# Performance work log

Measured on AMD Instinct MI355X. Metric: run time of the kernel, lower is better.

The kernel has to match this reference:

```python
import jax, jax.numpy as jnp
import numpy as np

N = 100000   # nodes
E = 1600000  # edges
F_IN = 64    # input features
H = 64       # hidden channels
C = 40       # classes


def setup_inputs() -> dict:
    key = jax.random.key(0)
    k1, k2, k3, k4 = jax.random.split(key, 4)
    x = jax.random.normal(k1, (N, F_IN), dtype=jnp.float32)
    edge_index = jax.random.randint(k2, (2, E), 0, N, dtype=jnp.int64)
    W1 = jax.random.normal(k3, (F_IN, H), dtype=jnp.float32) / np.sqrt(F_IN)
    b1 = jnp.zeros((H,), dtype=jnp.float32)
    W2 = jax.random.normal(k4, (H, C), dtype=jnp.float32) / np.sqrt(H)
    b2 = jnp.zeros((C,), dtype=jnp.float32)
    return {"x": x, "edge_index": edge_index, "W1": W1, "b1": b1, "W2": W2, "b2": b2}


def gcn_conv(x, src, dst, W, b):
    """PyG-style GCNConv: self-loops + symmetric deg^{-1/2} normalization.
    src/dst already include self-loops. x: [N, Fin], W: [Fin, Fout]."""
    n = x.shape[0]
    deg = jax.ops.segment_sum(jnp.ones_like(dst, dtype=x.dtype), dst, num_segments=n)
    dinv = jnp.where(deg > 0, jax.lax.rsqrt(deg), jnp.zeros_like(deg))
    norm = dinv[src] * dinv[dst]          # [E+N]
    h = x @ W                             # transform first (Fin -> Fout)
    msg = h[src] * norm[:, None]          # gather + scale, [E+N, Fout]
    out = jax.ops.segment_sum(msg, dst, num_segments=n)  # scatter-add
    return out + b


def reference(x, edge_index, W1, b1, W2, b2):
    n = x.shape[0]
    loops = jnp.arange(n, dtype=edge_index.dtype)
    src = jnp.concatenate([edge_index[0], loops])
    dst = jnp.concatenate([edge_index[1], loops])
    h = jax.nn.relu(gcn_conv(x, src, dst, W1, b1))
    # F.dropout in eval mode (training=False) is identity
    out = gcn_conv(h, src, dst, W2, b2)
    return jax.nn.log_softmax(out, axis=1)
```

## Files before the change

### kernel.cpp

```cpp
#include <hip/hip_runtime.h>
#include <math.h>

#define F1 64
#define F2 40
#define NB 1024
#define TILE 4096
#define FCAP 3200

typedef unsigned int uint;
typedef __attribute__((ext_vector_type(8))) short s8v;
typedef __attribute__((ext_vector_type(4))) float f4v;

union U8 { s8v s; uint4 q; uint u[4]; };

__device__ inline unsigned short f2bf(float f) {
    unsigned u = __float_as_uint(f);
    unsigned r = (u + 0x7FFFu + ((u >> 16) & 1u)) >> 16;
    return (unsigned short)r;
}
__device__ inline uint packbf(float lo, float hi) {
    return (uint)f2bf(lo) | ((uint)f2bf(hi) << 16);
}
__device__ inline float bf_lo(uint u) { return __uint_as_float(u << 16); }
__device__ inline float bf_hi(uint u) { return __uint_as_float(u & 0xFFFF0000u); }

__device__ inline void split2(float a, float b, uint* hu, uint* lu) {
    unsigned short ha = f2bf(a), hb = f2bf(b);
    *hu = (uint)ha | ((uint)hb << 16);
    float ra = a - __uint_as_float((uint)ha << 16);
    float rb = b - __uint_as_float((uint)hb << 16);
    *lu = packbf(ra, rb);
}

__global__ __launch_bounds__(256) void k_bhist(const int* __restrict__ dst,
                                               int* __restrict__ bcnt, int e, int bsh) {
    __shared__ int h[NB];
    int tid = threadIdx.x;
    for (int i = tid; i < NB; i += 256) h[i] = 0;
    __syncthreads();
    int base = blockIdx.x * TILE;
    int lim = min(base + TILE, e);
    for (int i = base + tid; i < lim; i += 256) atomicAdd(&h[dst[i] >> bsh], 1);
    __syncthreads();
    for (int i = tid; i < NB; i += 256) if (h[i]) atomicAdd(&bcnt[i], h[i]);
}

__global__ __launch_bounds__(NB) void k_bscan(const int* __restrict__ bcnt,
                                              int* __restrict__ bptr, int* __restrict__ gcur,
                                              int* __restrict__ row_ptr, int n, int e) {
    __shared__ int sh[NB];
    int t = threadIdx.x;
    sh[t] = bcnt[t];
    __syncthreads();
    for (int off = 1; off < NB; off <<= 1) {
        int v = (t >= off) ? sh[t - off] : 0;
        __syncthreads();
        sh[t] += v;
        __syncthreads();
    }
    int ex = t ? sh[t - 1] : 0;
    bptr[t] = ex;
    gcur[t] = ex;
    if (t == NB - 1) bptr[NB] = sh[NB - 1];
    if (t == 0) row_ptr[n] = e;
}

__global__ __launch_bounds__(256) void k_bscatter(const int* __restrict__ src,
                                                  const int* __restrict__ dst,
                                                  int* gcur,
                                                  unsigned long long* __restrict__ pairs,
                                                  int e, int bsh) {
    __shared__ int lhist[NB];
    __shared__ int lstart[NB];
    __shared__ int delta[NB];
    __shared__ unsigned long long stage[TILE];
    int tid = threadIdx.x;
    for (int i = tid; i < NB; i += 256) lhist[i] = 0;
    __syncthreads();
    int base = blockIdx.x * TILE;
    int cnt = min(TILE, e - base);
    int sA[16], dA[16], rA[16];
#pragma unroll
    for (int k = 0; k < 16; ++k) {
        int i = base + k * 256 + tid;
        if (i < e) {
            sA[k] = src[i];
            dA[k] = dst[i];
            rA[k] = atomicAdd(&lhist[dA[k] >> bsh], 1);
        }
    }
    __syncthreads();
    if (tid < 64) {
        const int per = NB / 64;
        int v[per];
        int b0 = tid * per, s = 0;
#pragma unroll
        for (int j = 0; j < per; ++j) { v[j] = lhist[b0 + j]; s += v[j]; }
        int sc = s;
        for (int o = 1; o < 64; o <<= 1) { int u = __shfl_up(sc, o); if (tid >= o) sc += u; }
        int ex = sc - s;
#pragma unroll
        for (int j = 0; j < per; ++j) { lstart[b0 + j] = ex; ex += v[j]; }
    }
    __syncthreads();
    for (int i = tid; i < NB; i += 256) {
        int c = lhist[i];
        if (c) delta[i] = atomicAdd(&gcur[i], c) - lstart[i];
    }
    __syncthreads();
#pragma unroll
    for (int k = 0; k < 16; ++k) {
        int i = base + k * 256 + tid;
        if (i < e) {
            int b = dA[k] >> bsh;
            stage[lstart[b] + rA[k]] =
                ((unsigned long long)(unsigned)sA[k] << 32) | (unsigned)dA[k];
        }
    }
    __syncthreads();
    for (int p = tid; p < cnt; p += 256) {
        unsigned long long pr = stage[p];
        int b = ((int)(unsigned)pr) >> bsh;
        pairs[delta[b] + p] = pr;
    }
}

__global__ __launch_bounds__(256) void k_final(const unsigned long long* __restrict__ pairs,
                                               const int* __restrict__ bptr,
                                               int* __restrict__ srcs,
                                               int* __restrict__ row_ptr,
                                               float* __restrict__ dinv,
                                               int n, int bsh) {
    __shared__ int ldeg[128];
    __shared__ int lrow[128];
    __shared__ int lcur[128];
    __shared__ unsigned long long stg[FCAP];
    int b = blockIdx.x, tid = threadIdx.x;
    int beg = bptr[b], cnt = bptr[b + 1] - beg;
    int node0 = b << bsh;
    int bnodes = 1 << bsh;
    for (int i = tid; i < bnodes; i += 256) { ldeg[i] = 0; lcur[i] = 0; }
    bool fit = cnt <= FCAP;
    __syncthreads();
    if (fit) {
        for (int p = tid; p < cnt; p += 256) {
            unsigned long long pr = pairs[beg + p];
            stg[p] = pr;
            atomicAdd(&ldeg[((int)(unsigned)pr) - node0], 1);
        }
    } else {
        for (int p = tid; p < cnt; p += 256)
            atomicAdd(&ldeg[((int)(unsigned)pairs[beg + p]) - node0], 1);
    }
    __syncthreads();
    if (tid < 64) {
        int per = bnodes >> 6;
        int b0 = tid * per, s = 0;
        for (int j = 0; j < per; ++j) s += ldeg[b0 + j];
        int sc = s;
        for (int o = 1; o < 64; o <<= 1) { int u = __shfl_up(sc, o); if (tid >= o) sc += u; }
        int ex = sc - s;
        for (int j = 0; j < per; ++j) { lrow[b0 + j] = ex; ex += ldeg[b0 + j]; }
    }
    __syncthreads();
    for (int i = tid; i < bnodes; i += 256) {
        int node = node0 + i;
        if (node < n) {
            row_ptr[node] = beg + lrow[i];
            dinv[node] = rsqrtf((float)(ldeg[i] + 1));
        }
    }
    if (fit) {
        for (int p = tid; p < cnt; p += 256) {
            unsigned long long pr = stg[p];
            int dl = ((int)(unsigned)pr) - node0;
            int r = atomicAdd(&lcur[dl], 1);
            srcs[beg + lrow[dl] + r] = (int)(pr >> 32);
        }
    } else {
        for (int p = tid; p < cnt; p += 256) {
            unsigned long long pr = pairs[beg + p];
            int dl = ((int)(unsigned)pr) - node0;
            int r = atomicAdd(&lcur[dl], 1);
            srcs[beg + lrow[dl] + r] = (int)(pr >> 32);
        }
    }
}

__global__ __launch_bounds__(256) void k_wprep(const float* __restrict__ W1,
                                               const float* __restrict__ W2,
                                               uint4* __restrict__ wf1,
                                               uint4* __restrict__ wf2) {
    int g = blockIdx.x * 256 + threadIdx.x;
    if (g < 512) {
        int ks = g >> 8, ct = (g >> 6) & 3, l = g & 63;
        int c = 16 * ct + (l & 15);
        int kb = 32 * ks + 8 * (l >> 4);
        uint hu[4], lu[4];
#pragma unroll
        for (int i = 0; i < 4; ++i)
            split2(W1[(kb + 2 * i) * 64 + c], W1[(kb + 2 * i + 1) * 64 + c], &hu[i], &lu[i]);
        wf1[(size_t)(ks * 4 + ct) * 64 + l]       = make_uint4(hu[0], hu[1], hu[2], hu[3]);
        wf1[(size_t)((2 + ks) * 4 + ct) * 64 + l] = make_uint4(lu[0], lu[1], lu[2], lu[3]);
    } else if (g < 896) {
        int v = g - 512;
        int ks = v / 192, rem = v % 192;
        int ct = rem >> 6, l = rem & 63;
        int c = 16 * ct + (l & 15);
        int kb = 32 * ks + 8 * (l >> 4);
        uint hu[4], lu[4];
#pragma unroll
        for (int i = 0; i < 4; ++i) {
            float a = (c < 40) ? W2[(kb + 2 * i) * 40 + c] : 0.0f;
            float b = (c < 40) ? W2[(kb + 2 * i + 1) * 40 + c] : 0.0f;
            split2(a, b, &hu[i], &lu[i]);
        }
        wf2[(size_t)(ks * 3 + ct) * 64 + l]       = make_uint4(hu[0], hu[1], hu[2], hu[3]);
        wf2[(size_t)((2 + ks) * 3 + ct) * 64 + l] = make_uint4(lu[0], lu[1], lu[2], lu[3]);
    }
}

__global__ __launch_bounds__(256) void k_gemm1(const float* __restrict__ x,
                                               const uint4* __restrict__ wf1,
                                               const float* __restrict__ dinv,
                                               unsigned short* __restrict__ h, int n) {
    int w = threadIdx.x >> 6, l = threadIdx.x & 63;
    int node0 = blockIdx.x * 64 + w * 16;
    int ar = min(node0 + (l & 15), n - 1);
    const float* ap = x + (size_t)ar * 64 + 8 * (l >> 4);
    float4 a0 = *(const float4*)ap;
    float4 a1 = *(const float4*)(ap + 4);
    float4 a2 = *(const float4*)(ap + 32);
    float4 a3 = *(const float4*)(ap + 36);
    U8 ah0, al0, ah1, al1;
    split2(a0.x, a0.y, &ah0.u[0], &al0.u[0]);
    split2(a0.z, a0.w, &ah0.u[1], &al0.u[1]);
    split2(a1.x, a1.y, &ah0.u[2], &al0.u[2]);
    split2(a1.z, a1.w, &ah0.u[3], &al0.u[3]);
    split2(a2.x, a2.y, &ah1.u[0], &al1.u[0]);
    split2(a2.z, a2.w, &ah1.u[1], &al1.u[1]);
    split2(a3.x, a3.y, &ah1.u[2], &al1.u[2]);
    split2(a3.z, a3.w, &ah1.u[3], &al1.u[3]);
    f4v acc[4];
#pragma unroll
    for (int ct = 0; ct < 4; ++ct) acc[ct] = (f4v){0.0f, 0.0f, 0.0f, 0.0f};
#pragma unroll
    for (int ct = 0; ct < 4; ++ct) {
        U8 bh0, bh1, bl0, bl1;
        bh0.q = wf1[(size_t)(0 * 4 + ct) * 64 + l];
        bh1.q = wf1[(size_t)(1 * 4 + ct) * 64 + l];
        bl0.q = wf1[(size_t)(2 * 4 + ct) * 64 + l];
        bl1.q = wf1[(size_t)(3 * 4 + ct) * 64 + l];
        acc[ct] = __builtin_amdgcn_mfma_f32_16x16x32_bf16(ah0.s, bh0.s, acc[ct], 0, 0, 0);
        acc[ct] = __builtin_amdgcn_mfma_f32_16x16x32_bf16(ah1.s, bh1.s, acc[ct], 0, 0, 0);
        acc[ct] = __builtin_amdgcn_mfma_f32_16x16x32_bf16(al0.s, bh0.s, acc[ct], 0, 0, 0);
        acc[ct] = __builtin_amdgcn_mfma_f32_16x16x32_bf16(al1.s, bh1.s, acc[ct], 0, 0, 0);
        acc[ct] = __builtin_amdgcn_mfma_f32_16x16x32_bf16(ah0.s, bl0.s, acc[ct], 0, 0, 0);
        acc[ct] = __builtin_amdgcn_mfma_f32_16x16x32_bf16(ah1.s, bl1.s, acc[ct], 0, 0, 0);
    }
    int r0 = node0 + (l >> 4) * 4;
    float dv[4];
#pragma unroll
    for (int r = 0; r < 4; ++r) dv[r] = dinv[min(r0 + r, n - 1)];
#pragma unroll
    for (int ct = 0; ct < 4; ++ct)
#pragma unroll
        for (int r = 0; r < 4; ++r)
            if (r0 + r < n)
                h[(size_t)(r0 + r) * 64 + 16 * ct + (l & 15)] = f2bf(acc[ct][r] * dv[r]);
}

__global__ __launch_bounds__(256) void k_gather(const uint4* __restrict__ h4,
                                                const int* __restrict__ srcs,
                                                const int* __restrict__ row_ptr,
                                                const float* __restrict__ dinv,
                                                const float* __restrict__ b,
                                                uint4* __restrict__ aggb, int n) {
    int node = (int)(((long long)blockIdx.x * 256 + threadIdx.x) >> 5);
    int lane = threadIdx.x & 63;
    int l32 = lane & 31;
    int hw = lane & 32;
    if (node >= n) return;
    int slot = l32 >> 3, j = l32 & 7;
    int e0 = row_ptr[node], cnt = row_ptr[node + 1] - e0;
    int idx = (l32 < cnt) ? srcs[e0 + l32] : 0;
    float a0x=0,a0y=0,a1x=0,a1y=0,a2x=0,a2y=0,a3x=0,a3y=0;
    if (slot == 0) {
        uint4 u = h4[(size_t)node * 8 + j];
        a0x = bf_lo(u.x); a0y = bf_hi(u.x);
        a1x = bf_lo(u.y); a1y = bf_hi(u.y);
        a2x = bf_lo(u.z); a2y = bf_hi(u.z);
        a3x = bf_lo(u.w); a3y = bf_hi(u.w);
    }
    int cl = max(min(cnt, 32) - 1, 0);
#pragma unroll
    for (int i = 0; i < 8; ++i) {
        int e = slot + 4 * i;
        int sv = __shfl(idx, hw + min(e, cl));
        uint4 u = h4[(size_t)sv * 8 + j];
        if (e < cnt) {
            a0x += bf_lo(u.x);  a0y += bf_hi(u.x);
            a1x += bf_lo(u.y);  a1y += bf_hi(u.y);
            a2x += bf_lo(u.z);  a2y += bf_hi(u.z);
            a3x += bf_lo(u.w);  a3y += bf_hi(u.w);
        }
    }
    for (int p = 32 + slot; p < cnt; p += 4) {
        int s0 = srcs[e0 + p];
        uint4 u0 = h4[(size_t)s0 * 8 + j];
        a0x += bf_lo(u0.x);  a0y += bf_hi(u0.x);
        a1x += bf_lo(u0.y);  a1y += bf_hi(u0.y);
        a2x += bf_lo(u0.z);  a2y += bf_hi(u0.z);
        a3x += bf_lo(u0.w);  a3y += bf_hi(u0.w);
    }
#define COMB(o) \
    a0x += __shfl_xor(a0x, o); a0y += __shfl_xor(a0y, o); \
    a1x += __shfl_xor(a1x, o); a1y += __shfl_xor(a1y, o); \
    a2x += __shfl_xor(a2x, o); a2y += __shfl_xor(a2y, o); \
    a3x += __shfl_xor(a3x, o); a3y += __shfl_xor(a3y, o);
    COMB(8) COMB(16)
#undef COMB
    if (slot == 0) {
        float di = dinv[node];
        float4 bl = *(const float4*)&b[8 * j];
        float4 bh = *(const float4*)&b[8 * j + 4];
        float v0 = fmaxf(fmaf(a0x, di, bl.x), 0.0f);
        float v1 = fmaxf(fmaf(a0y, di, bl.y), 0.0f);
        float v2 = fmaxf(fmaf(a1x, di, bl.z), 0.0f);
        float v3 = fmaxf(fmaf(a1y, di, bl.w), 0.0f);
        float v4 = fmaxf(fmaf(a2x, di, bh.x), 0.0f);
        float v5 = fmaxf(fmaf(a2y, di, bh.y), 0.0f);
        float v6 = fmaxf(fmaf(a3x, di, bh.z), 0.0f);
        float v7 = fmaxf(fmaf(a3y, di, bh.w), 0.0f);
        uint4 r;
        r.x = packbf(v0, v1); r.y = packbf(v2, v3);
        r.z = packbf(v4, v5); r.w = packbf(v6, v7);
        aggb[(size_t)node * 8 + j] = r;
    }
}

__global__ __launch_bounds__(256) void k_trans2(const uint4* __restrict__ aggb,
                                                const uint4* __restrict__ wf2,
                                                const float* __restrict__ dinv,
                                                unsigned short* __restrict__ t, int n) {
    int w = threadIdx.x >> 6, l = threadIdx.x & 63;
    int node0 = blockIdx.x * 64 + w * 16;
    int ar = min(node0 + (l & 15), n - 1);
    U8 a0, a1;
    a0.q = aggb[(size_t)ar * 8 + 0 + (l >> 4)];
    a1.q = aggb[(size_t)ar * 8 + 4 + (l >> 4)];
    f4v acc[3];
#pragma unroll
    for (int ct = 0; ct < 3; ++ct) acc[ct] = (f4v){0.0f, 0.0f, 0.0f, 0.0f};
#pragma unroll
    for (int ct = 0; ct < 3; ++ct) {
        U8 bh0, bh1, bl0, bl1;
        bh0.q = wf2[(size_t)(0 * 3 + ct) * 64 + l];
        bh1.q = wf2[(size_t)(1 * 3 + ct) * 64 + l];
        bl0.q = wf2[(size_t)(2 * 3 + ct) * 64 + l];
        bl1.q = wf2[(size_t)(3 * 3 + ct) * 64 + l];
        acc[ct] = __builtin_amdgcn_mfma_f32_16x16x32_bf16(a0.s, bh0.s, acc[ct], 0, 0, 0);
        acc[ct] = __builtin_amdgcn_mfma_f32_16x16x32_bf16(a1.s, bh1.s, acc[ct], 0, 0, 0);
        acc[ct] = __builtin_amdgcn_mfma_f32_16x16x32_bf16(a0.s, bl0.s, acc[ct], 0, 0, 0);
        acc[ct] = __builtin_amdgcn_mfma_f32_16x16x32_bf16(a1.s, bl1.s, acc[ct], 0, 0, 0);
    }
    int r0 = node0 + (l >> 4) * 4;
    float dv[4];
#pragma unroll
    for (int r = 0; r < 4; ++r) dv[r] = dinv[min(r0 + r, n - 1)];
#pragma unroll
    for (int ct = 0; ct < 3; ++ct) {
        int col = 16 * ct + (l & 15);
#pragma unroll
        for (int r = 0; r < 4; ++r)
            if (col < 40 && r0 + r < n)
                t[(size_t)(r0 + r) * 40 + col] = f2bf(acc[ct][r] * dv[r]);
    }
}

__global__ __launch_bounds__(256) void k_gather40(const uint2* __restrict__ t2,
                                                  const int* __restrict__ srcs,
                                                  const int* __restrict__ row_ptr,
                                                  const float* __restrict__ dinv,
                                                  const float* __restrict__ b2,
                                                  float* __restrict__ out, int n) {
    int node = (int)(((long long)blockIdx.x * 256 + threadIdx.x) >> 5);
    int lane = threadIdx.x & 63;
    int l32 = lane & 31;
    int hw = lane & 32;
    if (node >= n) return;
    int slot = l32 / 10;
    int j = l32 - slot * 10;
    int e0 = row_ptr[node];
    int cnt = row_ptr[node + 1] - e0;
    int idx = (l32 < cnt && l32 < 30) ? srcs[e0 + l32] : 0;
    float a0=0, a1=0, a2=0, a3=0;
    if (slot == 0) {
        uint2 u = t2[(size_t)node * 10 + j];
        a0 = bf_lo(u.x); a1 = bf_hi(u.x);
        a2 = bf_lo(u.y); a3 = bf_hi(u.y);
    }
    if (slot < 3) {
        int cl = max(min(cnt, 30) - 1, 0);
#pragma unroll
        for (int i = 0; i < 10; ++i) {
            int e = slot + 3 * i;
            int sv = __shfl(idx, hw + min(e, cl));
            uint2 u = t2[(size_t)sv * 10 + j];
            if (e < cnt) {
                a0 += bf_lo(u.x);  a1 += bf_hi(u.x);
                a2 += bf_lo(u.y);  a3 += bf_hi(u.y);
            }
        }
        for (int p = 30 + slot; p < cnt; p += 3) {
            int s0 = srcs[e0 + p];
            uint2 u0 = t2[(size_t)s0 * 10 + j];
            a0 += bf_lo(u0.x);  a1 += bf_hi(u0.x);
            a2 += bf_lo(u0.y);  a3 += bf_hi(u0.y);
        }
    }
    float t0 = a0 + __shfl(a0, lane + 10) + __shfl(a0, lane + 20);
    float t1 = a1 + __shfl(a1, lane + 10) + __shfl(a1, lane + 20);
    float t2s = a2 + __shfl(a2, lane + 10) + __shfl(a2, lane + 20);
    float t3 = a3 + __shfl(a3, lane + 10) + __shfl(a3, lane + 20);
    bool actc = l32 < 10;
    float di = dinv[node];
    float4 bb = actc ? *(const float4*)&b2[4 * l32] : make_float4(0, 0, 0, 0);
    float v0 = fmaf(t0, di, bb.x);
    float v1 = fmaf(t1, di, bb.y);
    float v2 = fmaf(t2s, di, bb.z);
    float v3 = fmaf(t3, di, bb.w);
    float mv = actc ? fmaxf(fmaxf(v0, v1), fmaxf(v2, v3)) : -INFINITY;
    for (int o = 16; o; o >>= 1) mv = fmaxf(mv, __shfl_xor(mv, o));
    float ex = actc ? (expf(v0 - mv) + expf(v1 - mv) + expf(v2 - mv) + expf(v3 - mv)) : 0.0f;
    float s = ex;
    for (int o = 16; o; o >>= 1) s += __shfl_xor(s, o);
    float ls = mv + logf(s);
    if (actc) {
        float4 r = make_float4(v0 - ls, v1 - ls, v2 - ls, v3 - ls);
        *(float4*)&out[(size_t)node * 40 + 4 * l32] = r;
    }
}

extern "C" void kernel_launch(void* const* d_in, const int* in_sizes, int n_in,
                              void* d_out, int out_size, void* d_ws, size_t ws_size,
                              hipStream_t stream) {
    const float* x  = (const float*)d_in[0];
    const int*   ei = (const int*)d_in[1];
    const float* W1 = (const float*)d_in[2];
    const float* b1 = (const float*)d_in[3];
    const float* W2 = (const float*)d_in[4];
    const float* b2 = (const float*)d_in[5];

    const int N = in_sizes[0] / F1;
    const int E = in_sizes[1] / 2;
    const int* src = ei;
    const int* dst = ei + E;

    int bsh = 7;
    while ((((N - 1) >> bsh) + 1) > NB) ++bsh;
    const int NBu = ((N - 1) >> bsh) + 1;

    uint4* h1b     = (uint4*)d_ws;
    uint4* aggb    = h1b + (size_t)N * 8;
    uint2* tb      = (uint2*)(aggb + (size_t)N * 8);
    uint4* wf1     = (uint4*)(tb + (size_t)N * 10);
    uint4* wf2     = wf1 + 1024;
    unsigned long long* pairs = (unsigned long long*)(wf2 + 768);
    int*   srcs    = (int*)(pairs + E);
    int*   row_ptr = srcs + E;
    float* dinv    = (float*)(row_ptr + N + 1);
    int*   bcnt    = (int*)(dinv + N);
    int*   bptr    = bcnt + NB;
    int*   gcur    = bptr + NB + 1;
    float* outp    = (float*)d_out;

    const int B = 256;
    const int GT = (E + TILE - 1) / TILE;

    k_wprep<<<4, B, 0, stream>>>(W1, W2, wf1, wf2);

    hipMemsetAsync(bcnt, 0, NB * sizeof(int), stream);
    k_bhist<<<GT, B, 0, stream>>>(dst, bcnt, E, bsh);
    k_bscan<<<1, NB, 0, stream>>>(bcnt, bptr, gcur, row_ptr, N, E);
    k_bscatter<<<GT, B, 0, stream>>>(src, dst, gcur, pairs, E, bsh);
    k_final<<<NBu, B, 0, stream>>>(pairs, bptr, srcs, row_ptr, dinv, N, bsh);

    const int GM = (N + 63) / 64;

    k_gemm1<<<GM, B, 0, stream>>>(x, wf1, dinv, (unsigned short*)h1b, N);
    k_gather<<<(N + 7) / 8, B, 0, stream>>>(h1b, srcs, row_ptr, dinv, b1, aggb, N);

    k_trans2<<<GM, B, 0, stream>>>(aggb, wf2, dinv, (unsigned short*)tb, N);
    k_gather40<<<(N + 7) / 8, B, 0, stream>>>(tb, srcs, row_ptr, dinv, b2, outp, N);
}
```

Before: 238.6 us.

## Replace two-pass bucket sort CSR build with atomic-degree counting scatter

The CSR construction no longer does a bucketed radix-style scatter of packed (src,dst) pairs followed by a per-bucket local sort. Instead, the histogram pass also counts per-node degree with global atomics, a small kernel computes row pointers and cursors per node, and a flat kernel places each source with a global atomicAdd on its destination cursor. This removes the 64-bit pairs buffer and a full extra read and write of the edge list. In exchange it adds about 1.6M global atomics on the degree pass and again on the scatter, writes into srcs in random order, and leaves neighbour order within a row nondeterministic, which can change the floating-point summation order.

```diff
diff --git a/kernel.cpp b/kernel.cpp
--- a/kernel.cpp
+++ b/kernel.cpp
@@ -5,7 +5,6 @@
 #define F2 40
 #define NB 1024
 #define TILE 4096
-#define FCAP 3200
 
 typedef unsigned int uint;
 typedef __attribute__((ext_vector_type(8))) short s8v;
@@ -32,21 +31,26 @@
     *lu = packbf(ra, rb);
 }
 
-__global__ __launch_bounds__(256) void k_bhist(const int* __restrict__ dst,
-                                               int* __restrict__ bcnt, int e, int bsh) {
+__global__ __launch_bounds__(256) void k_bhist2(const int* __restrict__ dst,
+                                                int* __restrict__ bcnt,
+                                                int* __restrict__ deg, int e, int bsh) {
     __shared__ int h[NB];
     int tid = threadIdx.x;
     for (int i = tid; i < NB; i += 256) h[i] = 0;
     __syncthreads();
     int base = blockIdx.x * TILE;
     int lim = min(base + TILE, e);
-    for (int i = base + tid; i < lim; i += 256) atomicAdd(&h[dst[i] >> bsh], 1);
+    for (int i = base + tid; i < lim; i += 256) {
+        int d = dst[i];
+        atomicAdd(&h[d >> bsh], 1);
+        atomicAdd(&deg[d], 1);
+    }
     __syncthreads();
     for (int i = tid; i < NB; i += 256) if (h[i]) atomicAdd(&bcnt[i], h[i]);
 }
 
 __global__ __launch_bounds__(NB) void k_bscan(const int* __restrict__ bcnt,
-                                              int* __restrict__ bptr, int* __restrict__ gcur,
+                                              int* __restrict__ bptr,
                                               int* __restrict__ row_ptr, int n, int e) {
     __shared__ int sh[NB];
     int t = threadIdx.x;
@@ -58,132 +62,50 @@
         sh[t] += v;
         __syncthreads();
     }
-    int ex = t ? sh[t - 1] : 0;
-    bptr[t] = ex;
-    gcur[t] = ex;
+    bptr[t] = t ? sh[t - 1] : 0;
     if (t == NB - 1) bptr[NB] = sh[NB - 1];
     if (t == 0) row_ptr[n] = e;
 }
 
-__global__ __launch_bounds__(256) void k_bscatter(const int* __restrict__ src,
-                                                  const int* __restrict__ dst,
-                                                  int* gcur,
-                                                  unsigned long long* __restrict__ pairs,
-                                                  int e, int bsh) {
-    __shared__ int lhist[NB];
-    __shared__ int lstart[NB];
-    __shared__ int delta[NB];
-    __shared__ unsigned long long stage[TILE];
-    int tid = threadIdx.x;
-    for (int i = tid; i < NB; i += 256) lhist[i] = 0;
-    __syncthreads();
-    int base = blockIdx.x * TILE;
-    int cnt = min(TILE, e - base);
-    int sA[16], dA[16], rA[16];
-#pragma unroll
-    for (int k = 0; k < 16; ++k) {
-        int i = base + k * 256 + tid;
-        if (i < e) {
-            sA[k] = src[i];
-            dA[k] = dst[i];
-            rA[k] = atomicAdd(&lhist[dA[k] >> bsh], 1);
-        }
-    }
+__global__ __launch_bounds__(128) void k_rowptr(const int* __restrict__ deg,
+                                                const int* __restrict__ bptr,
+                                                int* __restrict__ row_ptr,
+                                                int* __restrict__ cur,
+                                                float* __restrict__ dinv, int n, int bsh) {
+    __shared__ int ldeg[128];
+    __shared__ int lrow[128];
+    int b = blockIdx.x, tid = threadIdx.x;
+    int node0 = b << bsh;
+    int node = node0 + tid;
+    ldeg[tid] = (node < n) ? deg[node] : 0;
     __syncthreads();
     if (tid < 64) {
-        const int per = NB / 64;
-        int v[per];
-        int b0 = tid * per, s = 0;
-#pragma unroll
-        for (int j = 0; j < per; ++j) { v[j] = lhist[b0 + j]; s += v[j]; }
+        int v0 = ldeg[2 * tid], v1 = ldeg[2 * tid + 1];
+        int s = v0 + v1;
         int sc = s;
         for (int o = 1; o < 64; o <<= 1) { int u = __shfl_up(sc, o); if (tid >= o) sc += u; }
         int ex = sc - s;
-#pragma unroll
-        for (int j = 0; j < per; ++j) { lstart[b0 + j] = ex; ex += v[j]; }
+        lrow[2 * tid] = ex;
+        lrow[2 * tid + 1] = ex + v0;
     }
     __syncthreads();
-    for (int i = tid; i < NB; i += 256) {
-        int c = lhist[i];
-        if (c) delta[i] = atomicAdd(&gcur[i], c) - lstart[i];
-    }
-    __syncthreads();
-#pragma unroll
-    for (int k = 0; k < 16; ++k) {
-        int i = base + k * 256 + tid;
-        if (i < e) {
-            int b = dA[k] >> bsh;
-            stage[lstart[b] + rA[k]] =
-                ((unsigned long long)(unsigned)sA[k] << 32) | (unsigned)dA[k];
-        }
-    }
-    __syncthreads();
-    for (int p = tid; p < cnt; p += 256) {
-        unsigned long long pr = stage[p];
-        int b = ((int)(unsigned)pr) >> bsh;
-        pairs[delta[b] + p] = pr;
-    }
-}
-
-__global__ __launch_bounds__(256) void k_final(const unsigned long long* __restrict__ pairs,
-                                               const int* __restrict__ bptr,
-                                               int* __restrict__ srcs,
-                                               int* __restrict__ row_ptr,
-                                               float* __restrict__ dinv,
-                                               int n, int bsh) {
-    __shared__ int ldeg[128];
-    __shared__ int lrow[128];
-    __shared__ int lcur[128];
-    __shared__ unsigned long long stg[FCAP];
-    int b = blockIdx.x, tid = threadIdx.x;
-    int beg = bptr[b], cnt = bptr[b + 1] - beg;
-    int node0 = b << bsh;
-    int bnodes = 1 << bsh;
-    for (int i = tid; i < bnodes; i += 256) { ldeg[i] = 0; lcur[i] = 0; }
-    bool fit = cnt <= FCAP;
-    __syncthreads();
-    if (fit) {
-        for (int p = tid; p < cnt; p += 256) {
-            unsigned long long pr = pairs[beg + p];
-            stg[p] = pr;
-            atomicAdd(&ldeg[((int)(unsigned)pr) - node0], 1);
-        }
-    } else {
-        for (int p = tid; p < cnt; p += 256)
-            atomicAdd(&ldeg[((int)(unsigned)pairs[beg + p]) - node0], 1);
-    }
-    __syncthreads();
-    if (tid < 64) {
-        int per = bnodes >> 6;
-        int b0 = tid * per, s = 0;
-        for (int j = 0; j < per; ++j) s += ldeg[b0 + j];
-        int sc = s;
-        for (int o = 1; o < 64; o <<= 1) { int u = __shfl_up(sc, o); if (tid >= o) sc += u; }
-        int ex = sc - s;
-        for (int j = 0; j < per; ++j) { lrow[b0 + j] = ex; ex += ldeg[b0 + j]; }
-    }
-    __syncthreads();
-    for (int i = tid; i < bnodes; i += 256) {
-        int node = node0 + i;
-        if (node < n) {
-            row_ptr[node] = beg + lrow[i];
-            dinv[node] = rsqrtf((float)(ldeg[i] + 1));
-        }
-    }
-    if (fit) {
-        for (int p = tid; p < cnt; p += 256) {
-            unsigned long long pr = stg[p];
-            int dl = ((int)(unsigned)pr) - node0;
-            int r = atomicAdd(&lcur[dl], 1);
-            srcs[beg + lrow[dl] + r] = (int)(pr >> 32);
-        }
-    } else {
-        for (int p = tid; p < cnt; p += 256) {
-            unsigned long long pr = pairs[beg + p];
-            int dl = ((int)(unsigned)pr) - node0;
-            int r = atomicAdd(&lcur[dl], 1);
-            srcs[beg + lrow[dl] + r] = (int)(pr >> 32);
-        }
+    if (node < n) {
+        int rp = bptr[b] + lrow[tid];
+        row_ptr[node] = rp;
+        cur[node] = rp;
+        dinv[node] = rsqrtf((float)(ldeg[tid] + 1));
+    }
+}
+
+__global__ __launch_bounds__(256) void k_scatter(const int* __restrict__ src,
+                                                 const int* __restrict__ dst,
+                                                 int* __restrict__ cur,
+                                                 int* __restrict__ srcs, int e) {
+    int i = blockIdx.x * 256 + threadIdx.x;
+    if (i < e) {
+        int s = src[i], d = dst[i];
+        int pos = atomicAdd(&cur[d], 1);
+        srcs[pos] = s;
     }
 }
 
@@ -466,13 +388,13 @@
     uint2* tb      = (uint2*)(aggb + (size_t)N * 8);
     uint4* wf1     = (uint4*)(tb + (size_t)N * 10);
     uint4* wf2     = wf1 + 1024;
-    unsigned long long* pairs = (unsigned long long*)(wf2 + 768);
-    int*   srcs    = (int*)(pairs + E);
+    int*   srcs    = (int*)(wf2 + 768);
     int*   row_ptr = srcs + E;
     float* dinv    = (float*)(row_ptr + N + 1);
     int*   bcnt    = (int*)(dinv + N);
-    int*   bptr    = bcnt + NB;
-    int*   gcur    = bptr + NB + 1;
+    int*   deg     = bcnt + NB;
+    int*   cur     = deg + N;
+    int*   bptr    = cur + N;
     float* outp    = (float*)d_out;
 
     const int B = 256;
@@ -480,11 +402,11 @@
 
     k_wprep<<<4, B, 0, stream>>>(W1, W2, wf1, wf2);
 
-    hipMemsetAsync(bcnt, 0, NB * sizeof(int), stream);
-    k_bhist<<<GT, B, 0, stream>>>(dst, bcnt, E, bsh);
-    k_bscan<<<1, NB, 0, stream>>>(bcnt, bptr, gcur, row_ptr, N, E);
-    k_bscatter<<<GT, B, 0, stream>>>(src, dst, gcur, pairs, E, bsh);
-    k_final<<<NBu, B, 0, stream>>>(pairs, bptr, srcs, row_ptr, dinv, N, bsh);
+    hipMemsetAsync(bcnt, 0, (NB + N) * sizeof(int), stream);
+    k_bhist2<<<GT, B, 0, stream>>>(dst, bcnt, deg, E, bsh);
+    k_bscan<<<1, NB, 0, stream>>>(bcnt, bptr, row_ptr, N, E);
+    k_rowptr<<<NBu, 128, 0, stream>>>(deg, bptr, row_ptr, cur, dinv, N, bsh);
+    k_scatter<<<(E + B - 1) / B, B, 0, stream>>>(src, dst, cur, srcs, E);
 
     const int GM = (N + 63) / 64;
 
```

Result: slower. 375.7 us (+57.4%).

## Fuse layer-1 gather with layer-2 transform via shared-memory staging

Applied to the files above, without the earlier changes.

Merges the layer-1 neighbor aggregation kernel and the layer-2 MFMA transform into one kernel. Each 256-thread block now aggregates 64 nodes over 8 rounds into a padded LDS tile, then runs the bf16 MFMA against W2 directly from LDS. This removes the global write and re-read of the intermediate aggregate and one kernel launch. In exchange, each block does its gather serially over rounds with a barrier before the transform, and it has 8x fewer blocks, which may reduce memory-level parallelism for the latency-bound gather.

```diff
diff --git a/kernel.cpp b/kernel.cpp
--- a/kernel.cpp
+++ b/kernel.cpp
@@ -270,85 +270,89 @@
                 h[(size_t)(r0 + r) * 64 + 16 * ct + (l & 15)] = f2bf(acc[ct][r] * dv[r]);
 }
 
-__global__ __launch_bounds__(256) void k_gather(const uint4* __restrict__ h4,
-                                                const int* __restrict__ srcs,
-                                                const int* __restrict__ row_ptr,
-                                                const float* __restrict__ dinv,
-                                                const float* __restrict__ b,
-                                                uint4* __restrict__ aggb, int n) {
-    int node = (int)(((long long)blockIdx.x * 256 + threadIdx.x) >> 5);
-    int lane = threadIdx.x & 63;
+__global__ __launch_bounds__(256) void k_gat(const uint4* __restrict__ h4,
+                                             const int* __restrict__ srcs,
+                                             const int* __restrict__ row_ptr,
+                                             const float* __restrict__ dinv,
+                                             const float* __restrict__ b,
+                                             const uint4* __restrict__ wf2,
+                                             unsigned short* __restrict__ t, int n) {
+    __shared__ uint agg[64][36];
+    int tid = threadIdx.x;
+    int lane = tid & 63;
     int l32 = lane & 31;
     int hw = lane & 32;
-    if (node >= n) return;
     int slot = l32 >> 3, j = l32 & 7;
-    int e0 = row_ptr[node], cnt = row_ptr[node + 1] - e0;
-    int idx = (l32 < cnt) ? srcs[e0 + l32] : 0;
-    float a0x=0,a0y=0,a1x=0,a1y=0,a2x=0,a2y=0,a3x=0,a3y=0;
-    if (slot == 0) {
-        uint4 u = h4[(size_t)node * 8 + j];
-        a0x = bf_lo(u.x); a0y = bf_hi(u.x);
-        a1x = bf_lo(u.y); a1y = bf_hi(u.y);
-        a2x = bf_lo(u.z); a2y = bf_hi(u.z);
-        a3x = bf_lo(u.w); a3y = bf_hi(u.w);
-    }
-    int cl = max(min(cnt, 32) - 1, 0);
-#pragma unroll
-    for (int i = 0; i < 8; ++i) {
-        int e = slot + 4 * i;
-        int sv = __shfl(idx, hw + min(e, cl));
-        uint4 u = h4[(size_t)sv * 8 + j];
-        if (e < cnt) {
-            a0x += bf_lo(u.x);  a0y += bf_hi(u.x);
-            a1x += bf_lo(u.y);  a1y += bf_hi(u.y);
-            a2x += bf_lo(u.z);  a2y += bf_hi(u.z);
-            a3x += bf_lo(u.w);  a3y += bf_hi(u.w);
-        }
-    }
-    for (int p = 32 + slot; p < cnt; p += 4) {
-        int s0 = srcs[e0 + p];
-        uint4 u0 = h4[(size_t)s0 * 8 + j];
-        a0x += bf_lo(u0.x);  a0y += bf_hi(u0.x);
-        a1x += bf_lo(u0.y);  a1y += bf_hi(u0.y);
-        a2x += bf_lo(u0.z);  a2y += bf_hi(u0.z);
-        a3x += bf_lo(u0.w);  a3y += bf_hi(u0.w);
-    }
+    int nbase = blockIdx.x * 64;
+#pragma unroll 1
+    for (int rnd = 0; rnd < 8; ++rnd) {
+        int nl = rnd * 8 + (tid >> 5);
+        int node = nbase + nl;
+        if (node < n) {
+            int e0 = row_ptr[node], cnt = row_ptr[node + 1] - e0;
+            int idx = (l32 < cnt) ? srcs[e0 + l32] : 0;
+            float a0x=0,a0y=0,a1x=0,a1y=0,a2x=0,a2y=0,a3x=0,a3y=0;
+            if (slot == 0) {
+                uint4 u = h4[(size_t)node * 8 + j];
+                a0x = bf_lo(u.x); a0y = bf_hi(u.x);
+                a1x = bf_lo(u.y); a1y = bf_hi(u.y);
+                a2x = bf_lo(u.z); a2y = bf_hi(u.z);
+                a3x = bf_lo(u.w); a3y = bf_hi(u.w);
+            }
+            int cl = max(min(cnt, 32) - 1, 0);
+#pragma unroll
+            for (int i = 0; i < 8; ++i) {
+                int e = slot + 4 * i;
+                int sv = __shfl(idx, hw + min(e, cl));
+                uint4 u = h4[(size_t)sv * 8 + j];
+                if (e < cnt) {
+                    a0x += bf_lo(u.x);  a0y += bf_hi(u.x);
+                    a1x += bf_lo(u.y);  a1y += bf_hi(u.y);
+                    a2x += bf_lo(u.z);  a2y += bf_hi(u.z);
+                    a3x += bf_lo(u.w);  a3y += bf_hi(u.w);
+                }
+            }
+            for (int p = 32 + slot; p < cnt; p += 4) {
+                int s0 = srcs[e0 + p];
+                uint4 u0 = h4[(size_t)s0 * 8 + j];
+                a0x += bf_lo(u0.x);  a0y += bf_hi(u0.x);
+                a1x += bf_lo(u0.y);  a1y += bf_hi(u0.y);
+                a2x += bf_lo(u0.z);  a2y += bf_hi(u0.z);
+                a3x += bf_lo(u0.w);  a3y += bf_hi(u0.w);
+            }
 #define COMB(o) \
-    a0x += __shfl_xor(a0x, o); a0y += __shfl_xor(a0y, o); \
-    a1x += __shfl_xor(a1x, o); a1y += __shfl_xor(a1y, o); \
-    a2x += __shfl_xor(a2x, o); a2y += __shfl_xor(a2y, o); \
-    a3x += __shfl_xor(a3x, o); a3y += __shfl_xor(a3y, o);
-    COMB(8) COMB(16)
+            a0x += __shfl_xor(a0x, o); a0y += __shfl_xor(a0y, o); \
+            a1x += __shfl_xor(a1x, o); a1y += __shfl_xor(a1y, o); \
+            a2x += __shfl_xor(a2x, o); a2y += __shfl_xor(a2y, o); \
+            a3x += __shfl_xor(a3x, o); a3y += __shfl_xor(a3y, o);
+            COMB(8) COMB(16)
 #undef COMB
-    if (slot == 0) {
-        float di = dinv[node];
-        float4 bl = *(const float4*)&b[8 * j];
-        float4 bh = *(const float4*)&b[8 * j + 4];
-        float v0 = fmaxf(fmaf(a0x, di, bl.x), 0.0f);
-        float v1 = fmaxf(fmaf(a0y, di, bl.y), 0.0f);
-        float v2 = fmaxf(fmaf(a1x, di, bl.z), 0.0f);
-        float v3 = fmaxf(fmaf(a1y, di, bl.w), 0.0f);
-        float v4 = fmaxf(fmaf(a2x, di, bh.x), 0.0f);
-        float v5 = fmaxf(fmaf(a2y, di, bh.y), 0.0f);
-        float v6 = fmaxf(fmaf(a3x, di, bh.z), 0.0f);
-        float v7 = fmaxf(fmaf(a3y, di, bh.w), 0.0f);
-        uint4 r;
-        r.x = packbf(v0, v1); r.y = packbf(v2, v3);
-        r.z = packbf(v4, v5); r.w = packbf(v6, v7);
-        aggb[(size_t)node * 8 + j] = r;
-    }
-}
-
-__global__ __launch_bounds__(256) void k_trans2(const uint4* __restrict__ aggb,
-                                                const uint4* __restrict__ wf2,
-                                                const float* __restrict__ dinv,
-                                                unsigned short* __restrict__ t, int n) {
-    int w = threadIdx.x >> 6, l = threadIdx.x & 63;
-    int node0 = blockIdx.x * 64 + w * 16;
-    int ar = min(node0 + (l & 15), n - 1);
+            if (slot == 0) {
+                float di = dinv[node];
+                float4 bl = *(const float4*)&b[8 * j];
+                float4 bh = *(const float4*)&b[8 * j + 4];
+                float v0 = fmaxf(fmaf(a0x, di, bl.x), 0.0f);
+                float v1 = fmaxf(fmaf(a0y, di, bl.y), 0.0f);
+                float v2 = fmaxf(fmaf(a1x, di, bl.z), 0.0f);
+                float v3 = fmaxf(fmaf(a1y, di, bl.w), 0.0f);
+                float v4 = fmaxf(fmaf(a2x, di, bh.x), 0.0f);
+                float v5 = fmaxf(fmaf(a2y, di, bh.y), 0.0f);
+                float v6 = fmaxf(fmaf(a3x, di, bh.z), 0.0f);
+                float v7 = fmaxf(fmaf(a3y, di, bh.w), 0.0f);
+                uint4 r;
+                r.x = packbf(v0, v1); r.y = packbf(v2, v3);
+                r.z = packbf(v4, v5); r.w = packbf(v6, v7);
+                *(uint4*)&agg[nl][4 * j] = r;
+            }
+        }
+    }
+    __syncthreads();
+    int w = tid >> 6, l = tid & 63;
+    int node0 = nbase + w * 16;
+    int nl = w * 16 + (l & 15);
     U8 a0, a1;
-    a0.q = aggb[(size_t)ar * 8 + 0 + (l >> 4)];
-    a1.q = aggb[(size_t)ar * 8 + 4 + (l >> 4)];
+    a0.q = *(const uint4*)&agg[nl][4 * (l >> 4)];
+    a1.q = *(const uint4*)&agg[nl][16 + 4 * (l >> 4)];
     f4v acc[3];
 #pragma unroll
     for (int ct = 0; ct < 3; ++ct) acc[ct] = (f4v){0.0f, 0.0f, 0.0f, 0.0f};
@@ -462,8 +466,7 @@
     const int NBu = ((N - 1) >> bsh) + 1;
 
     uint4* h1b     = (uint4*)d_ws;
-    uint4* aggb    = h1b + (size_t)N * 8;
-    uint2* tb      = (uint2*)(aggb + (size_t)N * 8);
+    uint2* tb      = (uint2*)(h1b + (size_t)N * 8);
     uint4* wf1     = (uint4*)(tb + (size_t)N * 10);
     uint4* wf2     = wf1 + 1024;
     unsigned long long* pairs = (unsigned long long*)(wf2 + 768);
@@ -489,8 +492,8 @@
     const int GM = (N + 63) / 64;
 
     k_gemm1<<<GM, B, 0, stream>>>(x, wf1, dinv, (unsigned short*)h1b, N);
-    k_gather<<<(N + 7) / 8, B, 0, stream>>>(h1b, srcs, row_ptr, dinv, b1, aggb, N);
-
-    k_trans2<<<GM, B, 0, stream>>>(aggb, wf2, dinv, (unsigned short*)tb, N);
+    k_gat<<<GM, B, 0, stream>>>(h1b, srcs, row_ptr, dinv, b1, wf2,
+                                (unsigned short*)tb, N);
+
     k_gather40<<<(N + 7) / 8, B, 0, stream>>>(tb, srcs, row_ptr, dinv, b2, outp, N);
 }
```

After: 234.2 us. No clear change (-1.9%).
